# Optimization experiments

Hardware: AMD Instinct MI355X
Metric: run time of the kernel (lower is better)

The kernel has to match this reference:

```python
import jax, jax.numpy as jnp
import numpy as np
from jax import lax

K = 8  # dct_kernel_size

def _dct_matrix(n):
    m = np.zeros((n, n), dtype=np.float32)
    for k in range(n):
        for t in range(n):
            if k == 0:
                m[k, t] = 1.0 / np.sqrt(n)
            else:
                m[k, t] = np.sqrt(2.0 / n) * np.cos(np.pi * k * (2 * t + 1) / (2.0 * n))
    return jnp.asarray(m)

DCT = _dct_matrix(K)  # [8,8]


def setup_inputs() -> dict:
    key = jax.random.key(0)
    k1, k2, k3, k4, k5 = jax.random.split(key, 5)
    x = jax.random.normal(k1, (16, 1, 512, 512), dtype=jnp.float32)
    w1 = jax.random.normal(k2, (16, 1, 3, 3), dtype=jnp.float32) * 0.1
    b1 = jax.random.normal(k3, (16,), dtype=jnp.float32) * 0.01
    w2 = jax.random.normal(k4, (32, 16, 3, 3), dtype=jnp.float32) * 0.1
    b2 = jax.random.normal(k5, (32,), dtype=jnp.float32) * 0.01
    return {"x": x, "w1": w1, "b1": b1, "w2": w2, "b2": b2}


def _conv(x, w, b):
    y = lax.conv_general_dilated(x, w, (1, 1), 'SAME',
                                 dimension_numbers=('NCHW', 'OIHW', 'NCHW'))
    return y + b[None, :, None, None]


def reference(x, w1, b1, w2, b2):
    B, _, H, W = x.shape
    # non-overlapping 8x8 patches (equivalent to F.unfold k=stride=8)
    p = x.reshape(B, H // K, K, W // K, K).transpose(0, 1, 3, 2, 4)
    p = p.reshape(-1, K, K)                       # [P, 8, 8]
    # 2D DCT: DCT @ p @ DCT^T
    c = jnp.einsum('ij,pjk,lk->pil', DCT, p, DCT)  # [P, 8, 8]
    c = c[:, None]                                 # [P, 1, 8, 8]
    h = jax.nn.relu(_conv(c, w1, b1))              # [P, 16, 8, 8]
    h = _conv(h, w2, b2)                           # [P, 32, 8, 8]
    v = h.mean(axis=(2, 3))                        # adaptive avg pool -> [P, 32]
    C = v.shape[-1]
    return v.reshape(B, -1, C).mean(axis=1)        # [B, 32]
```

## Files before the change

kernel.cpp:

```cpp
#include <hip/hip_runtime.h>

namespace {

constexpr int IMGW = 512;
constexpr int NIMG = 16;
constexpr int C1N  = 16;
constexpr int C2N  = 32;
constexpr int NBLK = 1024;
constexpr int PART = C1N * 9;

constexpr float DCTM[8][8] = {
  {0.35355339059327373f, 0.35355339059327373f, 0.35355339059327373f, 0.35355339059327373f,
   0.35355339059327373f, 0.35355339059327373f, 0.35355339059327373f, 0.35355339059327373f},
  {0.49039264020161522f, 0.41573480615127262f, 0.27778511650980111f, 0.09754516100806413f,
  -0.09754516100806413f,-0.27778511650980111f,-0.41573480615127262f,-0.49039264020161522f},
  {0.46193976625564337f, 0.19134171618254492f,-0.19134171618254492f,-0.46193976625564337f,
  -0.46193976625564337f,-0.19134171618254492f, 0.19134171618254492f, 0.46193976625564337f},
  {0.41573480615127262f,-0.09754516100806413f,-0.49039264020161522f,-0.27778511650980111f,
   0.27778511650980111f, 0.49039264020161522f, 0.09754516100806413f,-0.41573480615127262f},
  {0.35355339059327373f,-0.35355339059327373f,-0.35355339059327373f, 0.35355339059327373f,
   0.35355339059327373f,-0.35355339059327373f,-0.35355339059327373f, 0.35355339059327373f},
  {0.27778511650980111f,-0.49039264020161522f, 0.09754516100806413f, 0.41573480615127262f,
  -0.41573480615127262f,-0.09754516100806413f, 0.49039264020161522f,-0.27778511650980111f},
  {0.19134171618254492f,-0.46193976625564337f, 0.46193976625564337f,-0.19134171618254492f,
  -0.19134171618254492f, 0.46193976625564337f,-0.46193976625564337f, 0.19134171618254492f},
  {0.09754516100806413f,-0.27778511650980111f, 0.41573480615127262f,-0.49039264020161522f,
   0.49039264020161522f,-0.41573480615127262f, 0.27778511650980111f,-0.09754516100806413f},
};

__global__ __launch_bounds__(256) void dct_conv_kernel(
    const float* __restrict__ x, const float* __restrict__ w1,
    const float* __restrict__ b1, float* __restrict__ partials)
{
  const int blk  = blockIdx.x;
  const int img  = blk >> 6;
  const int prow = blk & 63;
  const int lane = threadIdx.x & 63;
  const int wave = threadIdx.x >> 6;

  const float* base = x + ((size_t)img * IMGW + (size_t)prow * 8) * IMGW + (size_t)lane * 8;

  float p[8][8];
  #pragma unroll
  for (int r = 0; r < 8; ++r) {
    const float4 a = *reinterpret_cast<const float4*>(base + (size_t)r * IMGW);
    const float4 b = *reinterpret_cast<const float4*>(base + (size_t)r * IMGW + 4);
    p[r][0] = a.x; p[r][1] = a.y; p[r][2] = a.z; p[r][3] = a.w;
    p[r][4] = b.x; p[r][5] = b.y; p[r][6] = b.z; p[r][7] = b.w;
  }

  float t[8][8];
  #pragma unroll
  for (int i = 0; i < 8; ++i) {
    #pragma unroll
    for (int j = 0; j < 8; ++j) {
      float s = DCTM[i][0] * p[0][j];
      #pragma unroll
      for (int k = 1; k < 8; ++k) s = fmaf(DCTM[i][k], p[k][j], s);
      t[i][j] = s;
    }
  }
  float cf[8][8];
  #pragma unroll
  for (int i = 0; i < 8; ++i) {
    #pragma unroll
    for (int j = 0; j < 8; ++j) {
      float s = t[i][0] * DCTM[j][0];
      #pragma unroll
      for (int k = 1; k < 8; ++k) s = fmaf(t[i][k], DCTM[j][k], s);
      cf[i][j] = s;
    }
  }

  for (int cc = 0; cc < 4; ++cc) {
    const int ch = wave * 4 + cc;
    float w[9];
    #pragma unroll
    for (int q = 0; q < 9; ++q) w[q] = w1[ch * 9 + q];
    const float bb = b1[ch];

    float T = 0.f, R0 = 0.f, R7 = 0.f, Cs0 = 0.f, Cs7 = 0.f;
    float K00 = 0.f, K07 = 0.f, K70 = 0.f, K77 = 0.f;
    #pragma unroll
    for (int i = 0; i < 8; ++i) {
      #pragma unroll
      for (int j = 0; j < 8; ++j) {
        float a = bb;
        #pragma unroll
        for (int di = 0; di < 3; ++di) {
          const int ii = i + di - 1;
          if (ii >= 0 && ii < 8) {
            #pragma unroll
            for (int dj = 0; dj < 3; ++dj) {
              const int jj = j + dj - 1;
              if (jj >= 0 && jj < 8) a = fmaf(w[di * 3 + dj], cf[ii][jj], a);
            }
          }
        }
        a = fmaxf(a, 0.f);
        T += a;
        if (i == 0) R0 += a;
        if (i == 7) R7 += a;
        if (j == 0) Cs0 += a;
        if (j == 7) Cs7 += a;
        if (i == 0 && j == 0) K00 = a;
        if (i == 0 && j == 7) K07 = a;
        if (i == 7 && j == 0) K70 = a;
        if (i == 7 && j == 7) K77 = a;
      }
    }

    float v[9] = {T, R0, R7, Cs0, Cs7, K00, K07, K70, K77};
    #pragma unroll
    for (int q = 0; q < 9; ++q) {
      float s = v[q];
      #pragma unroll
      for (int m = 32; m >= 1; m >>= 1) s += __shfl_xor(s, m, 64);
      v[q] = s;
    }
    if (lane == 0) {
      #pragma unroll
      for (int q = 0; q < 9; ++q) partials[(size_t)blk * PART + ch * 9 + q] = v[q];
    }
  }
}

__global__ __launch_bounds__(192) void finish_kernel(
    const float* __restrict__ w2, const float* __restrict__ b2,
    const float* __restrict__ partials, float* __restrict__ out)
{
  const int img = blockIdx.x;
  const int tid = threadIdx.x;
  __shared__ float acc[C1N][9];
  if (tid < PART) {
    float s = 0.f;
    for (int k = 0; k < 64; ++k) s += partials[(size_t)(img * 64 + k) * PART + tid];
    acc[tid / 9][tid % 9] = s;
  }
  __syncthreads();
  if (tid < C2N) {
    float r = 0.f;
    for (int c1 = 0; c1 < C1N; ++c1) {
      const float T  = acc[c1][0], R0 = acc[c1][1], R7 = acc[c1][2];
      const float Q0 = acc[c1][3], Q7 = acc[c1][4];
      const float K00 = acc[c1][5], K07 = acc[c1][6], K70 = acc[c1][7], K77 = acc[c1][8];
      const float* wp = w2 + (size_t)(tid * C1N + c1) * 9;
      #pragma unroll
      for (int di = 0; di < 3; ++di) {
        #pragma unroll
        for (int dj = 0; dj < 3; ++dj) {
          float S = T;
          if (di == 0) S -= R7;
          if (di == 2) S -= R0;
          if (dj == 0) S -= Q7;
          if (dj == 2) S -= Q0;
          if (di == 0 && dj == 0) S += K77;
          if (di == 0 && dj == 2) S += K70;
          if (di == 2 && dj == 0) S += K07;
          if (di == 2 && dj == 2) S += K00;
          r = fmaf(wp[di * 3 + dj], S, r);
        }
      }
    }
    out[img * C2N + tid] = b2[tid] + r * (1.0f / 262144.0f);
  }
}

}

extern "C" void kernel_launch(void* const* d_in, const int* in_sizes, int n_in,
                              void* d_out, int out_size, void* d_ws, size_t ws_size,
                              hipStream_t stream) {
  const float* x  = (const float*)d_in[0];
  const float* w1 = (const float*)d_in[1];
  const float* b1 = (const float*)d_in[2];
  const float* w2 = (const float*)d_in[3];
  const float* b2 = (const float*)d_in[4];
  float* out      = (float*)d_out;
  float* partials = (float*)d_ws;

  dct_conv_kernel<<<NBLK, 256, 0, stream>>>(x, w1, b1, partials);
  finish_kernel<<<NIMG, 192, 0, stream>>>(w2, b2, partials, out);
}
```

Baseline: 35.80 us.

## Use fast butterfly DCT and process two patch rows per block

```diff
diff --git a/kernel.cpp b/kernel.cpp
--- a/kernel.cpp
+++ b/kernel.cpp
@@ -6,86 +6,59 @@
 constexpr int NIMG = 16;
 constexpr int C1N  = 16;
 constexpr int C2N  = 32;
-constexpr int NBLK = 1024;
+constexpr int NBLK = 512;
 constexpr int PART = C1N * 9;
 
-constexpr float DCTM[8][8] = {
-  {0.35355339059327373f, 0.35355339059327373f, 0.35355339059327373f, 0.35355339059327373f,
-   0.35355339059327373f, 0.35355339059327373f, 0.35355339059327373f, 0.35355339059327373f},
-  {0.49039264020161522f, 0.41573480615127262f, 0.27778511650980111f, 0.09754516100806413f,
-  -0.09754516100806413f,-0.27778511650980111f,-0.41573480615127262f,-0.49039264020161522f},
-  {0.46193976625564337f, 0.19134171618254492f,-0.19134171618254492f,-0.46193976625564337f,
-  -0.46193976625564337f,-0.19134171618254492f, 0.19134171618254492f, 0.46193976625564337f},
-  {0.41573480615127262f,-0.09754516100806413f,-0.49039264020161522f,-0.27778511650980111f,
-   0.27778511650980111f, 0.49039264020161522f, 0.09754516100806413f,-0.41573480615127262f},
-  {0.35355339059327373f,-0.35355339059327373f,-0.35355339059327373f, 0.35355339059327373f,
-   0.35355339059327373f,-0.35355339059327373f,-0.35355339059327373f, 0.35355339059327373f},
-  {0.27778511650980111f,-0.49039264020161522f, 0.09754516100806413f, 0.41573480615127262f,
-  -0.41573480615127262f,-0.09754516100806413f, 0.49039264020161522f,-0.27778511650980111f},
-  {0.19134171618254492f,-0.46193976625564337f, 0.46193976625564337f,-0.19134171618254492f,
-  -0.19134171618254492f, 0.46193976625564337f,-0.46193976625564337f, 0.19134171618254492f},
-  {0.09754516100806413f,-0.27778511650980111f, 0.41573480615127262f,-0.49039264020161522f,
-   0.49039264020161522f,-0.41573480615127262f, 0.27778511650980111f,-0.09754516100806413f},
-};
-
-__global__ __launch_bounds__(256) void dct_conv_kernel(
-    const float* __restrict__ x, const float* __restrict__ w1,
-    const float* __restrict__ b1, float* __restrict__ partials)
+__device__ __forceinline__ void dct8(const float x[8], float o[8]) {
+  const float c1 = 0.49039264020161522f;
+  const float c2 = 0.46193976625564337f;
+  const float c3 = 0.41573480615127262f;
+  const float c4 = 0.35355339059327373f;
+  const float c5 = 0.27778511650980111f;
+  const float c6 = 0.19134171618254492f;
+  const float c7 = 0.09754516100806413f;
+  const float s0 = x[0] + x[7], s1 = x[1] + x[6], s2 = x[2] + x[5], s3 = x[3] + x[4];
+  const float d0 = x[0] - x[7], d1 = x[1] - x[6], d2 = x[2] - x[5], d3 = x[3] - x[4];
+  const float e0 = s0 + s3, e1 = s1 + s2, e2 = s0 - s3, e3 = s1 - s2;
+  o[0] = c4 * (e0 + e1);
+  o[4] = c4 * (e0 - e1);
+  o[2] = fmaf(c2, e2,  c6 * e3);
+  o[6] = fmaf(c6, e2, -(c2 * e3));
+  o[1] = fmaf(c1, d0, fmaf( c3, d1, fmaf( c5, d2,  c7 * d3)));
+  o[3] = fmaf(c3, d0, fmaf(-c7, d1, fmaf(-c1, d2, -(c5 * d3))));
+  o[5] = fmaf(c5, d0, fmaf(-c1, d1, fmaf( c7, d2,  c3 * d3)));
+  o[7] = fmaf(c7, d0, fmaf(-c5, d1, fmaf( c3, d2, -(c1 * d3))));
+}
+
+__device__ __forceinline__ void process_patch(
+    const float p[8][8], const float w[4][9], const float bb[4], float acc[36])
 {
-  const int blk  = blockIdx.x;
-  const int img  = blk >> 6;
-  const int prow = blk & 63;
-  const int lane = threadIdx.x & 63;
-  const int wave = threadIdx.x >> 6;
-
-  const float* base = x + ((size_t)img * IMGW + (size_t)prow * 8) * IMGW + (size_t)lane * 8;
-
-  float p[8][8];
-  #pragma unroll
-  for (int r = 0; r < 8; ++r) {
-    const float4 a = *reinterpret_cast<const float4*>(base + (size_t)r * IMGW);
-    const float4 b = *reinterpret_cast<const float4*>(base + (size_t)r * IMGW + 4);
-    p[r][0] = a.x; p[r][1] = a.y; p[r][2] = a.z; p[r][3] = a.w;
-    p[r][4] = b.x; p[r][5] = b.y; p[r][6] = b.z; p[r][7] = b.w;
-  }
-
   float t[8][8];
   #pragma unroll
+  for (int j = 0; j < 8; ++j) {
+    float xin[8], xo[8];
+    #pragma unroll
+    for (int k = 0; k < 8; ++k) xin[k] = p[k][j];
+    dct8(xin, xo);
+    #pragma unroll
+    for (int k = 0; k < 8; ++k) t[k][j] = xo[k];
+  }
+  float cf[8][8];
+  #pragma unroll
   for (int i = 0; i < 8; ++i) {
-    #pragma unroll
-    for (int j = 0; j < 8; ++j) {
-      float s = DCTM[i][0] * p[0][j];
-      #pragma unroll
-      for (int k = 1; k < 8; ++k) s = fmaf(DCTM[i][k], p[k][j], s);
-      t[i][j] = s;
-    }
-  }
-  float cf[8][8];
-  #pragma unroll
-  for (int i = 0; i < 8; ++i) {
-    #pragma unroll
-    for (int j = 0; j < 8; ++j) {
-      float s = t[i][0] * DCTM[j][0];
-      #pragma unroll
-      for (int k = 1; k < 8; ++k) s = fmaf(t[i][k], DCTM[j][k], s);
-      cf[i][j] = s;
-    }
-  }
-
+    float xo[8];
+    dct8(t[i], xo);
+    #pragma unroll
+    for (int k = 0; k < 8; ++k) cf[i][k] = xo[k];
+  }
+
+  #pragma unroll
   for (int cc = 0; cc < 4; ++cc) {
-    const int ch = wave * 4 + cc;
-    float w[9];
-    #pragma unroll
-    for (int q = 0; q < 9; ++q) w[q] = w1[ch * 9 + q];
-    const float bb = b1[ch];
-
-    float T = 0.f, R0 = 0.f, R7 = 0.f, Cs0 = 0.f, Cs7 = 0.f;
-    float K00 = 0.f, K07 = 0.f, K70 = 0.f, K77 = 0.f;
     #pragma unroll
     for (int i = 0; i < 8; ++i) {
       #pragma unroll
       for (int j = 0; j < 8; ++j) {
-        float a = bb;
+        float a = bb[cc];
         #pragma unroll
         for (int di = 0; di < 3; ++di) {
           const int ii = i + di - 1;
@@ -93,35 +66,83 @@
             #pragma unroll
             for (int dj = 0; dj < 3; ++dj) {
               const int jj = j + dj - 1;
-              if (jj >= 0 && jj < 8) a = fmaf(w[di * 3 + dj], cf[ii][jj], a);
+              if (jj >= 0 && jj < 8) a = fmaf(w[cc][di * 3 + dj], cf[ii][jj], a);
             }
           }
         }
         a = fmaxf(a, 0.f);
-        T += a;
-        if (i == 0) R0 += a;
-        if (i == 7) R7 += a;
-        if (j == 0) Cs0 += a;
-        if (j == 7) Cs7 += a;
-        if (i == 0 && j == 0) K00 = a;
-        if (i == 0 && j == 7) K07 = a;
-        if (i == 7 && j == 0) K70 = a;
-        if (i == 7 && j == 7) K77 = a;
+        acc[cc * 9 + 0] += a;
+        if (i == 0) acc[cc * 9 + 1] += a;
+        if (i == 7) acc[cc * 9 + 2] += a;
+        if (j == 0) acc[cc * 9 + 3] += a;
+        if (j == 7) acc[cc * 9 + 4] += a;
+        if (i == 0 && j == 0) acc[cc * 9 + 5] += a;
+        if (i == 0 && j == 7) acc[cc * 9 + 6] += a;
+        if (i == 7 && j == 0) acc[cc * 9 + 7] += a;
+        if (i == 7 && j == 7) acc[cc * 9 + 8] += a;
       }
     }
-
-    float v[9] = {T, R0, R7, Cs0, Cs7, K00, K07, K70, K77};
-    #pragma unroll
-    for (int q = 0; q < 9; ++q) {
-      float s = v[q];
+  }
+}
+
+__global__ __launch_bounds__(256, 2) void dct_conv_kernel(
+    const float* __restrict__ x, const float* __restrict__ w1,
+    const float* __restrict__ b1, float* __restrict__ partials)
+{
+  const int blk  = blockIdx.x;
+  const int img  = blk >> 5;
+  const int pr2  = (blk & 31) * 2;
+  const int lane = threadIdx.x & 63;
+  const int wave = threadIdx.x >> 6;
+
+  const float* base0 = x + ((size_t)img * IMGW + (size_t)pr2 * 8) * IMGW + (size_t)lane * 8;
+  const float* base1 = base0 + (size_t)8 * IMGW;
+
+  float p0[8][8], p1[8][8];
+  #pragma unroll
+  for (int r = 0; r < 8; ++r) {
+    const float4 a = *reinterpret_cast<const float4*>(base0 + (size_t)r * IMGW);
+    const float4 b = *reinterpret_cast<const float4*>(base0 + (size_t)r * IMGW + 4);
+    p0[r][0] = a.x; p0[r][1] = a.y; p0[r][2] = a.z; p0[r][3] = a.w;
+    p0[r][4] = b.x; p0[r][5] = b.y; p0[r][6] = b.z; p0[r][7] = b.w;
+  }
+  #pragma unroll
+  for (int r = 0; r < 8; ++r) {
+    const float4 a = *reinterpret_cast<const float4*>(base1 + (size_t)r * IMGW);
+    const float4 b = *reinterpret_cast<const float4*>(base1 + (size_t)r * IMGW + 4);
+    p1[r][0] = a.x; p1[r][1] = a.y; p1[r][2] = a.z; p1[r][3] = a.w;
+    p1[r][4] = b.x; p1[r][5] = b.y; p1[r][6] = b.z; p1[r][7] = b.w;
+  }
+
+  float w[4][9], bb[4];
+  #pragma unroll
+  for (int cc = 0; cc < 4; ++cc) {
+    const int ch = wave * 4 + cc;
+    #pragma unroll
+    for (int q = 0; q < 9; ++q) w[cc][q] = w1[ch * 9 + q];
+    bb[cc] = b1[ch];
+  }
+
+  float acc[36];
+  #pragma unroll
+  for (int q = 0; q < 36; ++q) acc[q] = 0.f;
+
+  process_patch(p0, w, bb, acc);
+  process_patch(p1, w, bb, acc);
+
+  #pragma unroll
+  for (int q = 0; q < 36; ++q) {
+    float s = acc[q];
+    #pragma unroll
+    for (int m = 32; m >= 1; m >>= 1) s += __shfl_xor(s, m, 64);
+    acc[q] = s;
+  }
+  if (lane == 0) {
+    #pragma unroll
+    for (int cc = 0; cc < 4; ++cc)
       #pragma unroll
-      for (int m = 32; m >= 1; m >>= 1) s += __shfl_xor(s, m, 64);
-      v[q] = s;
-    }
-    if (lane == 0) {
-      #pragma unroll
-      for (int q = 0; q < 9; ++q) partials[(size_t)blk * PART + ch * 9 + q] = v[q];
-    }
+      for (int q = 0; q < 9; ++q)
+        partials[(size_t)blk * PART + (wave * 4 + cc) * 9 + q] = acc[cc * 9 + q];
   }
 }
 
@@ -134,7 +155,7 @@
   __shared__ float acc[C1N][9];
   if (tid < PART) {
     float s = 0.f;
-    for (int k = 0; k < 64; ++k) s += partials[(size_t)(img * 64 + k) * PART + tid];
+    for (int k = 0; k < 32; ++k) s += partials[(size_t)(img * 32 + k) * PART + tid];
     acc[tid / 9][tid % 9] = s;
   }
   __syncthreads();
```

New measurement: 106.3 us. 197% more time.

## Fold DCT and conv1 into a precomputed matrix and run it on MFMA

Applied to the files above, without the earlier changes.

```diff
diff --git a/kernel.cpp b/kernel.cpp
--- a/kernel.cpp
+++ b/kernel.cpp
@@ -2,14 +2,15 @@
 
 namespace {
 
-constexpr int IMGW = 512;
 constexpr int NIMG = 16;
 constexpr int C1N  = 16;
 constexpr int C2N  = 32;
-constexpr int NBLK = 1024;
 constexpr int PART = C1N * 9;
 
-constexpr float DCTM[8][8] = {
+typedef __attribute__((ext_vector_type(8)))  _Float16 half8;
+typedef __attribute__((ext_vector_type(16))) float    f32x16;
+
+__device__ const float DCTM[8][8] = {
   {0.35355339059327373f, 0.35355339059327373f, 0.35355339059327373f, 0.35355339059327373f,
    0.35355339059327373f, 0.35355339059327373f, 0.35355339059327373f, 0.35355339059327373f},
   {0.49039264020161522f, 0.41573480615127262f, 0.27778511650980111f, 0.09754516100806413f,
@@ -28,114 +29,165 @@
    0.49039264020161522f,-0.41573480615127262f, 0.27778511650980111f,-0.09754516100806413f},
 };
 
-__global__ __launch_bounds__(256) void dct_conv_kernel(
-    const float* __restrict__ x, const float* __restrict__ w1,
-    const float* __restrict__ b1, float* __restrict__ partials)
+__global__ __launch_bounds__(256) void setup_M(
+    const float* __restrict__ w1, const float* __restrict__ b1,
+    _Float16* __restrict__ Mf)
 {
-  const int blk  = blockIdx.x;
-  const int img  = blk >> 6;
-  const int prow = blk & 63;
-  const int lane = threadIdx.x & 63;
-  const int wave = threadIdx.x >> 6;
-
-  const float* base = x + ((size_t)img * IMGW + (size_t)prow * 8) * IMGW + (size_t)lane * 8;
-
-  float p[8][8];
+  const int f = blockIdx.x * 256 + threadIdx.x;
+  if (f >= 32 * 5 * 64) return;
+  const int l  = f & 63;
+  const int rc = f >> 6;
+  const int c  = rc % 5;
+  const int rt = rc / 5;
+  const int ch = rt >> 1;
+  const int hi = l >> 5;
+  const int s  = (rt & 1) * 32 + (l & 31);
+  const int i = s >> 3, j = s & 7;
+
+  half8 e;
+  if (c == 4) {
+    #pragma unroll
+    for (int b = 0; b < 8; ++b) e[b] = (_Float16)0.f;
+    if (hi == 0) e[0] = (_Float16)b1[ch];
+  } else {
+    #pragma unroll
+    for (int b = 0; b < 8; ++b) {
+      const int k = c * 16 + hi * 8 + b;
+      const int u = k >> 3, v = k & 7;
+      float acc = 0.f;
+      for (int di = 0; di < 3; ++di) {
+        const int ii = i + di - 1;
+        if (ii < 0 || ii > 7) continue;
+        for (int dj = 0; dj < 3; ++dj) {
+          const int jj = j + dj - 1;
+          if (jj < 0 || jj > 7) continue;
+          acc = fmaf(w1[ch * 9 + di * 3 + dj], DCTM[ii][u] * DCTM[jj][v], acc);
+        }
+      }
+      e[b] = (_Float16)acc;
+    }
+  }
+  *reinterpret_cast<half8*>(Mf + (size_t)f * 8) = e;
+}
+
+__global__ __launch_bounds__(64, 2) void gemm_kernel(
+    const float* __restrict__ x, const _Float16* __restrict__ Mf,
+    float* __restrict__ partials)
+{
+  const int bid   = blockIdx.x;
+  const int slice = bid >> 9;
+  const int g     = bid & 511;
+  const int img   = g >> 5, gi = g & 31;
+  const int lane  = threadIdx.x;
+  const int col   = lane & 31, hi = lane >> 5;
+
+  half8 bfrag[4][4];
   #pragma unroll
-  for (int r = 0; r < 8; ++r) {
-    const float4 a = *reinterpret_cast<const float4*>(base + (size_t)r * IMGW);
-    const float4 b = *reinterpret_cast<const float4*>(base + (size_t)r * IMGW + 4);
-    p[r][0] = a.x; p[r][1] = a.y; p[r][2] = a.z; p[r][3] = a.w;
-    p[r][4] = b.x; p[r][5] = b.y; p[r][6] = b.z; p[r][7] = b.w;
-  }
-
-  float t[8][8];
+  for (int ct = 0; ct < 4; ++ct) {
+    const int prow = 2 * gi + (ct >> 1);
+    const int pcol = (ct & 1) * 32 + col;
+    const float* pb = x + (((size_t)img * 512 + (size_t)prow * 8) * 512 + (size_t)pcol * 8);
+    #pragma unroll
+    for (int m = 0; m < 4; ++m) {
+      const int u = 2 * m + hi;
+      const float4 lo = *reinterpret_cast<const float4*>(pb + (size_t)u * 512);
+      const float4 h4 = *reinterpret_cast<const float4*>(pb + (size_t)u * 512 + 4);
+      half8 h;
+      h[0] = (_Float16)lo.x; h[1] = (_Float16)lo.y; h[2] = (_Float16)lo.z; h[3] = (_Float16)lo.w;
+      h[4] = (_Float16)h4.x; h[5] = (_Float16)h4.y; h[6] = (_Float16)h4.z; h[7] = (_Float16)h4.w;
+      bfrag[ct][m] = h;
+    }
+  }
+  const float hm0 = (hi == 0) ? 1.f : 0.f;
+  const float hm1 = 1.f - hm0;
+  half8 bones;
   #pragma unroll
-  for (int i = 0; i < 8; ++i) {
-    #pragma unroll
-    for (int j = 0; j < 8; ++j) {
-      float s = DCTM[i][0] * p[0][j];
+  for (int b = 0; b < 8; ++b) bones[b] = (_Float16)0.f;
+  bones[0] = (_Float16)hm0;
+
+  #pragma unroll 1
+  for (int cc = 0; cc < 4; ++cc) {
+    float t_ = 0.f, r0 = 0.f, r7 = 0.f, c0 = 0.f, c7 = 0.f;
+    float k00 = 0.f, k07 = 0.f, k70 = 0.f, k77 = 0.f;
+    #pragma unroll
+    for (int rp = 0; rp < 2; ++rp) {
+      const int rtg = slice * 8 + cc * 2 + rp;
+      const _Float16* ap = Mf + ((size_t)(rtg * 5) * 64 + (size_t)lane) * 8;
+      const half8 a0 = *reinterpret_cast<const half8*>(ap);
+      const half8 a1 = *reinterpret_cast<const half8*>(ap + 512);
+      const half8 a2 = *reinterpret_cast<const half8*>(ap + 1024);
+      const half8 a3 = *reinterpret_cast<const half8*>(ap + 1536);
+      const half8 a4 = *reinterpret_cast<const half8*>(ap + 2048);
       #pragma unroll
-      for (int k = 1; k < 8; ++k) s = fmaf(DCTM[i][k], p[k][j], s);
-      t[i][j] = s;
-    }
-  }
-  float cf[8][8];
-  #pragma unroll
-  for (int i = 0; i < 8; ++i) {
-    #pragma unroll
-    for (int j = 0; j < 8; ++j) {
-      float s = t[i][0] * DCTM[j][0];
+      for (int ct = 0; ct < 4; ++ct) {
+        f32x16 d;
+        #pragma unroll
+        for (int r = 0; r < 16; ++r) d[r] = 0.f;
+        d = __builtin_amdgcn_mfma_f32_32x32x16_f16(a0, bfrag[ct][0], d, 0, 0, 0);
+        d = __builtin_amdgcn_mfma_f32_32x32x16_f16(a1, bfrag[ct][1], d, 0, 0, 0);
+        d = __builtin_amdgcn_mfma_f32_32x32x16_f16(a2, bfrag[ct][2], d, 0, 0, 0);
+        d = __builtin_amdgcn_mfma_f32_32x32x16_f16(a3, bfrag[ct][3], d, 0, 0, 0);
+        d = __builtin_amdgcn_mfma_f32_32x32x16_f16(a4, bones,        d, 0, 0, 0);
+
+        float v[16];
+        #pragma unroll
+        for (int r = 0; r < 16; ++r) v[r] = fmaxf(d[r], 0.f);
+        const float q0 = (v[0]  + v[1])  + (v[2]  + v[3]);
+        const float q1 = (v[4]  + v[5])  + (v[6]  + v[7]);
+        const float q2 = (v[8]  + v[9])  + (v[10] + v[11]);
+        const float q3 = (v[12] + v[13]) + (v[14] + v[15]);
+        t_ += (q0 + q1) + (q2 + q3);
+        if (rp == 0) {
+          r0 += q0;
+          k00 = fmaf(hm0, v[0],  k00);
+          k07 = fmaf(hm1, v[3],  k07);
+        } else {
+          r7 += q3;
+          k70 = fmaf(hm0, v[12], k70);
+          k77 = fmaf(hm1, v[15], k77);
+        }
+        c0 = fmaf(hm0, (v[0] + v[4]) + (v[8]  + v[12]), c0);
+        c7 = fmaf(hm1, (v[3] + v[7]) + (v[11] + v[15]), c7);
+      }
+    }
+    float vv[9] = {t_, r0, r7, c0, c7, k00, k07, k70, k77};
+    #pragma unroll
+    for (int q = 0; q < 9; ++q) {
+      float s = vv[q];
+      s += __shfl_xor(s, 1); s += __shfl_xor(s, 2);
+      s += __shfl_xor(s, 4); s += __shfl_xor(s, 8);
+      vv[q] = s;
+    }
+    if ((lane & 15) == 0) {
+      const size_t prw = (size_t)g * 4 + (lane >> 4);
+      float* dst = partials + prw * PART + (size_t)(slice * 4 + cc) * 9;
       #pragma unroll
-      for (int k = 1; k < 8; ++k) s = fmaf(t[i][k], DCTM[j][k], s);
-      cf[i][j] = s;
-    }
-  }
-
-  for (int cc = 0; cc < 4; ++cc) {
-    const int ch = wave * 4 + cc;
-    float w[9];
-    #pragma unroll
-    for (int q = 0; q < 9; ++q) w[q] = w1[ch * 9 + q];
-    const float bb = b1[ch];
-
-    float T = 0.f, R0 = 0.f, R7 = 0.f, Cs0 = 0.f, Cs7 = 0.f;
-    float K00 = 0.f, K07 = 0.f, K70 = 0.f, K77 = 0.f;
-    #pragma unroll
-    for (int i = 0; i < 8; ++i) {
-      #pragma unroll
-      for (int j = 0; j < 8; ++j) {
-        float a = bb;
-        #pragma unroll
-        for (int di = 0; di < 3; ++di) {
-          const int ii = i + di - 1;
-          if (ii >= 0 && ii < 8) {
-            #pragma unroll
-            for (int dj = 0; dj < 3; ++dj) {
-              const int jj = j + dj - 1;
-              if (jj >= 0 && jj < 8) a = fmaf(w[di * 3 + dj], cf[ii][jj], a);
-            }
-          }
-        }
-        a = fmaxf(a, 0.f);
-        T += a;
-        if (i == 0) R0 += a;
-        if (i == 7) R7 += a;
-        if (j == 0) Cs0 += a;
-        if (j == 7) Cs7 += a;
-        if (i == 0 && j == 0) K00 = a;
-        if (i == 0 && j == 7) K07 = a;
-        if (i == 7 && j == 0) K70 = a;
-        if (i == 7 && j == 7) K77 = a;
-      }
-    }
-
-    float v[9] = {T, R0, R7, Cs0, Cs7, K00, K07, K70, K77};
-    #pragma unroll
-    for (int q = 0; q < 9; ++q) {
-      float s = v[q];
-      #pragma unroll
-      for (int m = 32; m >= 1; m >>= 1) s += __shfl_xor(s, m, 64);
-      v[q] = s;
-    }
-    if (lane == 0) {
-      #pragma unroll
-      for (int q = 0; q < 9; ++q) partials[(size_t)blk * PART + ch * 9 + q] = v[q];
-    }
-  }
-}
-
-__global__ __launch_bounds__(192) void finish_kernel(
+      for (int q = 0; q < 9; ++q) dst[q] = vv[q];
+    }
+  }
+}
+
+__global__ __launch_bounds__(576) void finish_kernel(
     const float* __restrict__ w2, const float* __restrict__ b2,
     const float* __restrict__ partials, float* __restrict__ out)
 {
-  const int img = blockIdx.x;
-  const int tid = threadIdx.x;
+  const int img  = blockIdx.x;
+  const int tid  = threadIdx.x;
+  const int comp = tid % PART;
+  const int chnk = tid / PART;
+
+  __shared__ float part[4][PART];
   __shared__ float acc[C1N][9];
+
+  {
+    float s = 0.f;
+    const float* pb = partials + ((size_t)img * 128 + (size_t)chnk * 32) * PART + comp;
+    for (int k = 0; k < 32; ++k) s += pb[(size_t)k * PART];
+    part[chnk][comp] = s;
+  }
+  __syncthreads();
   if (tid < PART) {
-    float s = 0.f;
-    for (int k = 0; k < 64; ++k) s += partials[(size_t)(img * 64 + k) * PART + tid];
-    acc[tid / 9][tid % 9] = s;
+    acc[tid / 9][tid % 9] = (part[0][tid] + part[1][tid]) + (part[2][tid] + part[3][tid]);
   }
   __syncthreads();
   if (tid < C2N) {
@@ -177,8 +229,11 @@
   const float* w2 = (const float*)d_in[3];
   const float* b2 = (const float*)d_in[4];
   float* out      = (float*)d_out;
-  float* partials = (float*)d_ws;
-
-  dct_conv_kernel<<<NBLK, 256, 0, stream>>>(x, w1, b1, partials);
-  finish_kernel<<<NIMG, 192, 0, stream>>>(w2, b2, partials, out);
-}
+
+  _Float16* Mf    = (_Float16*)d_ws;
+  float* partials = (float*)((char*)d_ws + 262144);
+
+  setup_M<<<40, 256, 0, stream>>>(w1, b1, Mf);
+  gemm_kernel<<<2048, 64, 0, stream>>>(x, Mf, partials);
+  finish_kernel<<<NIMG, 576, 0, stream>>>(w2, b2, partials, out);
+}
```

New measurement: 31.55 us. 11.9% less time.
